# Optimization experiments

Measured on AMD Instinct MI355X. Metric: run time of the kernel, lower is better.

## Reference

```python
import jax, jax.numpy as jnp
import numpy as np

N_MOTIF_PER_CLASS = 8
N_CLASS = 16
N_MOTIF = N_MOTIF_PER_CLASS * N_CLASS
TEMPERATURE = 0.2
TAU = 0.99
K2 = 32
EPS = 1e-4


def setup_inputs() -> dict:
    key = jax.random.key(0)
    k1, k2, k3 = jax.random.split(key, 3)
    N, H = 32768, 1024
    z = jax.random.normal(k1, (N, H), dtype=jnp.float32)
    Motif_Vector = jax.random.normal(k2, (N_MOTIF, H), dtype=jnp.float32)
    y = jax.random.randint(k3, (N,), 0, N_CLASS, dtype=jnp.int64)
    return {"z": z, "Motif_Vector": Motif_Vector, "y": y}


def euclidean_1(X, M):
    # squared euclidean distance via GEMM, then log-ratio similarity
    xp = X @ M.T                                     # [N, n_motif]
    distance = (-2.0 * xp
                + jnp.sum(X * X, axis=1, keepdims=True)
                + jnp.sum(M * M, axis=1)[None, :])
    similarity = jnp.log((distance + 1.0) / (distance + EPS))
    return similarity, distance


def reference(z, Motif_Vector, y):
    similarity, distance = euclidean_1(z, Motif_Vector)

    # mapping: motif j belongs to class j // n_motif_per_class
    motif_class = jnp.arange(N_MOTIF) // N_MOTIF_PER_CLASS   # [n_motif]
    true_motifs = (y[:, None] == motif_class[None, :])       # [N, n_motif]

    # contrastive loss (exact torch math: exp(sim/T), max over positives,
    # sum over negatives)
    sims = jnp.exp(similarity / TEMPERATURE)
    sim_pos = jnp.max(jnp.where(true_motifs, sims, -jnp.inf), axis=1)
    sim_neg_sum = jnp.sum(jnp.where(true_motifs, 0.0, sims), axis=1)
    loss = -jnp.mean(jnp.log(sim_pos / (sim_neg_sum + sim_pos)))

    # update_motif (update_type='topk', weighted_mean=False):
    # torch passes `distance` into filter_similar_graph and argsorts
    # descending, i.e. selects the K2 LARGEST distances among same-class
    # samples (faithful to source).
    masked = jnp.where(true_motifs.T, distance.T, -jnp.inf)  # [n_motif, N]
    _, idx = jax.lax.top_k(masked, K2)                       # [n_motif, K2]
    selected = z[idx]                                        # [n_motif, K2, H]
    new_motif = jnp.mean(selected, axis=1)                   # weights = 1/K2
    new_M = TAU * Motif_Vector + (1.0 - TAU) * new_motif

    return loss, new_M
```

## Files before the change

kernel.cpp:

```cpp
#include <hip/hip_runtime.h>
#include <cstdint>
#include <cmath>

#define NROWS 32768
#define HD    1024
#define NMOT  128
#define NCLS  16
#define KSEL  32
#define EPSV  1e-4f

typedef __attribute__((ext_vector_type(4))) float  f32x4;
typedef __attribute__((ext_vector_type(8))) __bf16 bf16x8;
typedef __attribute__((ext_vector_type(4))) __bf16 bf16x4;
typedef unsigned long long u64;

#define WS_MN   64
#define WS_MVBF 256
#define WS_CD   65792
#define WS_S1K  327936
#define WS_CL   459008
#define WS_CCNT 524544
#define CAPC    256

static __device__ __forceinline__ float dot4(float4 v) {
    return v.x * v.x + v.y * v.y + v.z * v.z + v.w * v.w;
}

static __device__ __forceinline__ bf16x4 cvt4(float4 v) {
    bf16x4 t;
    t[0] = (__bf16)v.x; t[1] = (__bf16)v.y; t[2] = (__bf16)v.z; t[3] = (__bf16)v.w;
    return t;
}

static __device__ __forceinline__ u64 pack_key(float v, int idx) {
    unsigned int b = __float_as_uint(v);
    unsigned int mo = (b & 0x80000000u) ? ~b : (b | 0x80000000u);
    unsigned int khi = ~mo;
    return ((u64)khi << 32) | (unsigned int)idx;
}

__global__ __launch_bounds__(256) void prep_k(const float* __restrict__ mv,
                                              const int* __restrict__ y,
                                              float* __restrict__ wsf,
                                              __bf16* __restrict__ mvbf,
                                              int* __restrict__ clist,
                                              int* __restrict__ ccnt) {
    const int b = blockIdx.x;
    const int tid = threadIdx.x;
    if (b < NMOT) {
        const int k = tid * 4;
        float4 v = *(const float4*)&mv[(size_t)b * HD + k];
        *(bf16x4*)&mvbf[(size_t)b * HD + k] = cvt4(v);
        float s = dot4(v);
#pragma unroll
        for (int o = 1; o < 64; o <<= 1) s += __shfl_xor(s, o, 64);
        __shared__ float red[4];
        if ((tid & 63) == 0) red[tid >> 6] = s;
        __syncthreads();
        if (tid == 0) {
            wsf[WS_MN + b] = red[0] + red[1] + red[2] + red[3];
            if (b == 0) wsf[0] = 0.f;
        }
    } else {
        __shared__ int cnt;
        const int lid = b - NMOT;
        const int cls = lid >> 4, chunk = lid & 15;
        const int lane = tid & 63;
        if (tid == 0) cnt = 0;
        __syncthreads();
        const int base = chunk * 2048;
#pragma unroll
        for (int t = 0; t < 8; ++t) {
            const int i = base + t * 256 + tid;
            const bool pred = (y[i] == cls);
            const u64 m = __ballot(pred);
            int wbase = 0;
            if (lane == 0 && m) wbase = atomicAdd(&cnt, (int)__popcll(m));
            wbase = __shfl(wbase, 0, 64);
            if (pred) {
                const int p = wbase + (int)__popcll(m & ((1ull << lane) - 1ull));
                if (p < CAPC) clist[lid * CAPC + p] = i;
            }
        }
        __syncthreads();
        if (tid == 0) ccnt[lid] = cnt < CAPC ? cnt : CAPC;
    }
}

#define BM 64
#define BN 128
#define BK 32
#define NS (HD / BK)
#define SA 40

__global__ __launch_bounds__(256, 2) void gemm_fused(
    const float* __restrict__ z, const __bf16* __restrict__ mvbf,
    const float* __restrict__ mn, float* __restrict__ cd,
    const int* __restrict__ y, float* __restrict__ lossAcc) {
    __shared__ __bf16 As[2][BM * SA];
    __shared__ __bf16 Bs[2][BN * SA];
    __shared__ float  szn[BM];
    __shared__ int    ly[BM];
    __shared__ float  spm[2][BM];
    __shared__ float  sns[2][BM];

    const int tid  = threadIdx.x;
    const int row0 = blockIdx.x * BM;
    const int lane = tid & 63;
    const int wave = tid >> 6;
    const int wr   = wave >> 1;
    const int wc   = wave & 1;
    const int l15  = lane & 15;
    const int quad = lane >> 4;

    const int sq = tid & 7;
    const int sr = tid >> 3;
    const int bq = tid & 3;
    const int br = tid >> 2;

    if (tid < BM) ly[tid] = y[row0 + tid];

    f32x4 acc[2][4];
#pragma unroll
    for (int i = 0; i < 2; ++i)
#pragma unroll
        for (int j = 0; j < 4; ++j) acc[i][j] = (f32x4){0.f, 0.f, 0.f, 0.f};

    float zsq0 = 0.f, zsq1 = 0.f;

    const float*  zb = z + (size_t)(row0 + sr) * HD + sq * 4;
    const __bf16* bb = mvbf + (size_t)br * HD + bq * 8;

    float4 ra0[4], ra1[4];
    bf16x8 rb0[4], rb1[4];
#pragma unroll
    for (int s = 0; s < 4; ++s) {
        ra0[s] = *(const float4*)(zb + s * BK);
        ra1[s] = *(const float4*)(zb + s * BK + 32 * HD);
        rb0[s] = *(const bf16x8*)(bb + s * BK);
        rb1[s] = *(const bf16x8*)(bb + s * BK + 64 * HD);
    }
    *(bf16x4*)&As[0][sr * SA + sq * 4]        = cvt4(ra0[0]);
    *(bf16x4*)&As[0][(sr + 32) * SA + sq * 4] = cvt4(ra1[0]);
    *(bf16x8*)&Bs[0][br * SA + bq * 8]        = rb0[0];
    *(bf16x8*)&Bs[0][(br + 64) * SA + bq * 8] = rb1[0];
    zsq0 += dot4(ra0[0]); zsq1 += dot4(ra1[0]);
    ra0[0] = *(const float4*)(zb + 4 * BK);
    ra1[0] = *(const float4*)(zb + 4 * BK + 32 * HD);
    rb0[0] = *(const bf16x8*)(bb + 4 * BK);
    rb1[0] = *(const bf16x8*)(bb + 4 * BK + 64 * HD);
    __syncthreads();

    for (int it = 0; it < NS / 4; ++it) {
#pragma unroll
        for (int u = 0; u < 4; ++u) {
            const int kt = it * 4 + u;
            const int rbuf = kt & 1;
            const int ko = quad * 8;
            bf16x8 af[2], bfr[4];
#pragma unroll
            for (int i = 0; i < 2; ++i)
                af[i] = *(const bf16x8*)&As[rbuf][(wr * 32 + i * 16 + l15) * SA + ko];
#pragma unroll
            for (int j = 0; j < 4; ++j)
                bfr[j] = *(const bf16x8*)&Bs[rbuf][(wc * 64 + j * 16 + l15) * SA + ko];
            if (kt + 1 < NS) {
                const int w = (kt + 1) & 1;
                const int s = (kt + 1) & 3;
                *(bf16x4*)&As[w][sr * SA + sq * 4]        = cvt4(ra0[s]);
                *(bf16x4*)&As[w][(sr + 32) * SA + sq * 4] = cvt4(ra1[s]);
                *(bf16x8*)&Bs[w][br * SA + bq * 8]        = rb0[s];
                *(bf16x8*)&Bs[w][(br + 64) * SA + bq * 8] = rb1[s];
                zsq0 += dot4(ra0[s]); zsq1 += dot4(ra1[s]);
                if (kt + 5 < NS) {
                    const float*  zn = zb + (kt + 5) * BK;
                    const __bf16* bn = bb + (kt + 5) * BK;
                    ra0[s] = *(const float4*)(zn);
                    ra1[s] = *(const float4*)(zn + 32 * HD);
                    rb0[s] = *(const bf16x8*)(bn);
                    rb1[s] = *(const bf16x8*)(bn + 64 * HD);
                }
            }
#pragma unroll
            for (int i = 0; i < 2; ++i)
#pragma unroll
                for (int j = 0; j < 4; ++j)
                    acc[i][j] = __builtin_amdgcn_mfma_f32_16x16x32_bf16(
                        af[i], bfr[j], acc[i][j], 0, 0, 0);
            __syncthreads();
        }
    }

#pragma unroll
    for (int o = 1; o < 8; o <<= 1) {
        zsq0 += __shfl_xor(zsq0, o, 64);
        zsq1 += __shfl_xor(zsq1, o, 64);
    }
    if (sq == 0) { szn[sr] = zsq0; szn[sr + 32] = zsq1; }
    __syncthreads();

    f32x4 znv[2];
    int rcls[2][4];
#pragma unroll
    for (int i = 0; i < 2; ++i) {
        znv[i] = *(const f32x4*)&szn[wr * 32 + i * 16 + quad * 4];
#pragma unroll
        for (int reg = 0; reg < 4; ++reg)
            rcls[i][reg] = ly[wr * 32 + i * 16 + quad * 4 + reg];
    }
    float pm[2][4], ns[2][4];
#pragma unroll
    for (int i = 0; i < 2; ++i)
#pragma unroll
        for (int reg = 0; reg < 4; ++reg) { pm[i][reg] = 0.f; ns[i][reg] = 0.f; }

#pragma unroll
    for (int j = 0; j < 4; ++j) {
        const int c = wc * 64 + j * 16 + l15;
        const float mc = mn[c];
        const int ccls = c >> 3;
#pragma unroll
        for (int i = 0; i < 2; ++i) {
#pragma unroll
            for (int reg = 0; reg < 4; ++reg) {
                const int row = wr * 32 + i * 16 + quad * 4 + reg;
                float d = znv[i][reg] + mc - 2.f * acc[i][j][reg];
                float r = (d + 1.0f) * __builtin_amdgcn_rcpf(d + EPSV);
                float r2 = r * r;
                float s = r2 * r2 * r;
                if (ccls == rcls[i][reg]) {
                    pm[i][reg] = fmaxf(pm[i][reg], s);
                    cd[(size_t)(row0 + row) * 8 + (c & 7)] = d;
                } else {
                    ns[i][reg] += s;
                }
            }
        }
    }
#pragma unroll
    for (int o = 1; o < 16; o <<= 1) {
#pragma unroll
        for (int i = 0; i < 2; ++i)
#pragma unroll
            for (int reg = 0; reg < 4; ++reg) {
                pm[i][reg] = fmaxf(pm[i][reg], __shfl_xor(pm[i][reg], o, 64));
                ns[i][reg] += __shfl_xor(ns[i][reg], o, 64);
            }
    }
    if (l15 == 0) {
#pragma unroll
        for (int i = 0; i < 2; ++i)
#pragma unroll
            for (int reg = 0; reg < 4; ++reg) {
                const int row = wr * 32 + i * 16 + quad * 4 + reg;
                spm[wc][row] = pm[i][reg];
                sns[wc][row] = ns[i][reg];
            }
    }
    __syncthreads();
    if (tid < BM) {
        float p = fmaxf(spm[0][tid], spm[1][tid]);
        float nsum = sns[0][tid] + sns[1][tid];
        float li = logf((nsum + p) / p);
#pragma unroll
        for (int o = 1; o < 64; o <<= 1) li += __shfl_xor(li, o, 64);
        if (tid == 0) atomicAdd(lossAcc, li);
    }
}

__global__ __launch_bounds__(256) void sel1_k(const int* __restrict__ clist,
                                              const int* __restrict__ ccnt,
                                              const float* __restrict__ cd,
                                              u64* __restrict__ s1k) {
    __shared__ u64 keys[256];

    const int bid = blockIdx.x;
    const int j = bid >> 4, chunk = bid & 15;
    const int cls = j >> 3, m8 = j & 7;
    const int lid = cls * 16 + chunk;
    const int tid = threadIdx.x;

    const int n = ccnt[lid];
    u64 key = ~0ull;
    if (tid < n) {
        const int idx = clist[lid * CAPC + tid];
        key = pack_key(cd[(size_t)idx * 8 + m8], idx);
    }
    keys[tid] = key;
    __syncthreads();

    for (int k = 2; k <= 256; k <<= 1) {
        for (int jj = k >> 1; jj > 0; jj >>= 1) {
            if (tid < 128) {
                const int i  = ((tid & ~(jj - 1)) << 1) | (tid & (jj - 1));
                const int ix = i | jj;
                const u64 A = keys[i], B = keys[ix];
                const bool up = ((i & k) == 0);
                if ((A > B) == up) { keys[i] = B; keys[ix] = A; }
            }
            __syncthreads();
        }
    }
    if (tid < KSEL) s1k[(size_t)j * 512 + chunk * KSEL + tid] = keys[tid];
}

__global__ __launch_bounds__(256) void merge_k(
    const float* __restrict__ z, const float* __restrict__ mv,
    const u64* __restrict__ s1k, const float* __restrict__ lossAcc,
    float* __restrict__ out) {
    __shared__ u64 keys[512];
    __shared__ int sel[KSEL];

    const int b = blockIdx.x;
    const int j = b >> 2, q = b & 3;
    const int tid = threadIdx.x;
    keys[tid]       = s1k[(size_t)j * 512 + tid];
    keys[tid + 256] = s1k[(size_t)j * 512 + 256 + tid];
    __syncthreads();

    for (int k = 2; k <= 512; k <<= 1) {
        for (int jj = k >> 1; jj > 0; jj >>= 1) {
            const int i  = ((tid & ~(jj - 1)) << 1) | (tid & (jj - 1));
            const int ix = i | jj;
            const u64 A = keys[i], B = keys[ix];
            const bool up = ((i & k) == 0);
            if ((A > B) == up) { keys[i] = B; keys[ix] = A; }
            __syncthreads();
        }
    }
    if (tid < KSEL) sel[tid] = (int)(keys[tid] & 0xFFFFFFFFu);
    __syncthreads();

    const int h = q * 256 + tid;
    float s = 0.f;
#pragma unroll 8
    for (int r = 0; r < KSEL; ++r) s += z[(size_t)sel[r] * HD + h];
    out[1 + (size_t)j * HD + h] =
        0.99f * mv[(size_t)j * HD + h] + 0.01f * (s * (1.0f / KSEL));
    if (b == 0 && tid == 0) out[0] = lossAcc[0] * (1.0f / NROWS);
}

extern "C" void kernel_launch(void* const* d_in, const int* in_sizes, int n_in,
                              void* d_out, int out_size, void* d_ws, size_t ws_size,
                              hipStream_t stream) {
    const float* z  = (const float*)d_in[0];
    const float* mv = (const float*)d_in[1];
    const int*   y  = (const int*)d_in[2];
    float* out = (float*)d_out;
    float* wsf = (float*)d_ws;
    float*  mn    = wsf + WS_MN;
    __bf16* mvbf  = (__bf16*)(wsf + WS_MVBF);
    float*  cd    = wsf + WS_CD;
    u64*    s1k   = (u64*)(wsf + WS_S1K);
    int*    clist = (int*)(wsf + WS_CL);
    int*    ccnt  = (int*)(wsf + WS_CCNT);

    hipLaunchKernelGGL(prep_k,     dim3(NMOT + 256), dim3(256), 0, stream,
                       mv, y, wsf, mvbf, clist, ccnt);
    hipLaunchKernelGGL(gemm_fused, dim3(NROWS / BM), dim3(256), 0, stream,
                       z, mvbf, mn, cd, y, wsf);
    hipLaunchKernelGGL(sel1_k,     dim3(NMOT * 16),  dim3(256), 0, stream,
                       clist, ccnt, cd, s1k);
    hipLaunchKernelGGL(merge_k,    dim3(NMOT * 4),   dim3(256), 0, stream,
                       z, mv, s1k, wsf, out);
}
```

Baseline: 231.0 us.

## Fuse prep, selection and merge kernels into two launches with last-block merge

Removes the prep kernel: the GEMM now reads fp32 motif vectors directly, converting them to bf16 in-loop and computing motif norms itself. Class-list building moves into the selection kernel, and the final merge is done by the last-arriving block per motif via an atomic counter. The loss is reduced deterministically from per-block partials instead of a global atomic. This cuts launches from four to two, at the cost of every GEMM block redundantly converting and normalising the full motif matrix, plus 16x redundant y scans in the selection kernel.

```diff
diff --git a/kernel.cpp b/kernel.cpp
--- a/kernel.cpp
+++ b/kernel.cpp
@@ -14,12 +14,10 @@
 typedef __attribute__((ext_vector_type(4))) __bf16 bf16x4;
 typedef unsigned long long u64;
 
-#define WS_MN   64
-#define WS_MVBF 256
-#define WS_CD   65792
-#define WS_S1K  327936
-#define WS_CL   459008
-#define WS_CCNT 524544
+#define WS_LP   0
+#define WS_MC   512
+#define WS_S1K  1024
+#define WS_CD   132096
 #define CAPC    256
 
 static __device__ __forceinline__ float dot4(float4 v) {
@@ -29,6 +27,13 @@
 static __device__ __forceinline__ bf16x4 cvt4(float4 v) {
     bf16x4 t;
     t[0] = (__bf16)v.x; t[1] = (__bf16)v.y; t[2] = (__bf16)v.z; t[3] = (__bf16)v.w;
+    return t;
+}
+
+static __device__ __forceinline__ bf16x8 cvt8(float4 a, float4 b) {
+    bf16x8 t;
+    t[0] = (__bf16)a.x; t[1] = (__bf16)a.y; t[2] = (__bf16)a.z; t[3] = (__bf16)a.w;
+    t[4] = (__bf16)b.x; t[5] = (__bf16)b.y; t[6] = (__bf16)b.z; t[7] = (__bf16)b.w;
     return t;
 }
 
@@ -39,54 +44,6 @@
     return ((u64)khi << 32) | (unsigned int)idx;
 }
 
-__global__ __launch_bounds__(256) void prep_k(const float* __restrict__ mv,
-                                              const int* __restrict__ y,
-                                              float* __restrict__ wsf,
-                                              __bf16* __restrict__ mvbf,
-                                              int* __restrict__ clist,
-                                              int* __restrict__ ccnt) {
-    const int b = blockIdx.x;
-    const int tid = threadIdx.x;
-    if (b < NMOT) {
-        const int k = tid * 4;
-        float4 v = *(const float4*)&mv[(size_t)b * HD + k];
-        *(bf16x4*)&mvbf[(size_t)b * HD + k] = cvt4(v);
-        float s = dot4(v);
-#pragma unroll
-        for (int o = 1; o < 64; o <<= 1) s += __shfl_xor(s, o, 64);
-        __shared__ float red[4];
-        if ((tid & 63) == 0) red[tid >> 6] = s;
-        __syncthreads();
-        if (tid == 0) {
-            wsf[WS_MN + b] = red[0] + red[1] + red[2] + red[3];
-            if (b == 0) wsf[0] = 0.f;
-        }
-    } else {
-        __shared__ int cnt;
-        const int lid = b - NMOT;
-        const int cls = lid >> 4, chunk = lid & 15;
-        const int lane = tid & 63;
-        if (tid == 0) cnt = 0;
-        __syncthreads();
-        const int base = chunk * 2048;
-#pragma unroll
-        for (int t = 0; t < 8; ++t) {
-            const int i = base + t * 256 + tid;
-            const bool pred = (y[i] == cls);
-            const u64 m = __ballot(pred);
-            int wbase = 0;
-            if (lane == 0 && m) wbase = atomicAdd(&cnt, (int)__popcll(m));
-            wbase = __shfl(wbase, 0, 64);
-            if (pred) {
-                const int p = wbase + (int)__popcll(m & ((1ull << lane) - 1ull));
-                if (p < CAPC) clist[lid * CAPC + p] = i;
-            }
-        }
-        __syncthreads();
-        if (tid == 0) ccnt[lid] = cnt < CAPC ? cnt : CAPC;
-    }
-}
-
 #define BM 64
 #define BN 128
 #define BK 32
@@ -94,12 +51,13 @@
 #define SA 40
 
 __global__ __launch_bounds__(256, 2) void gemm_fused(
-    const float* __restrict__ z, const __bf16* __restrict__ mvbf,
-    const float* __restrict__ mn, float* __restrict__ cd,
-    const int* __restrict__ y, float* __restrict__ lossAcc) {
+    const float* __restrict__ z, const float* __restrict__ mv,
+    float* __restrict__ cd, const int* __restrict__ y,
+    float* __restrict__ lossP, int* __restrict__ mcnt) {
     __shared__ __bf16 As[2][BM * SA];
     __shared__ __bf16 Bs[2][BN * SA];
     __shared__ float  szn[BM];
+    __shared__ float  smn[BN];
     __shared__ int    ly[BM];
     __shared__ float  spm[2][BM];
     __shared__ float  sns[2][BM];
@@ -118,6 +76,7 @@
     const int bq = tid & 3;
     const int br = tid >> 2;
 
+    if (blockIdx.x == 0 && tid < NMOT) mcnt[tid] = 0;
     if (tid < BM) ly[tid] = y[row0 + tid];
 
     f32x4 acc[2][4];
@@ -127,28 +86,38 @@
         for (int j = 0; j < 4; ++j) acc[i][j] = (f32x4){0.f, 0.f, 0.f, 0.f};
 
     float zsq0 = 0.f, zsq1 = 0.f;
-
-    const float*  zb = z + (size_t)(row0 + sr) * HD + sq * 4;
-    const __bf16* bb = mvbf + (size_t)br * HD + bq * 8;
+    float msq0 = 0.f, msq1 = 0.f;
+
+    const float* zb = z  + (size_t)(row0 + sr) * HD + sq * 4;
+    const float* bb = mv + (size_t)br * HD + bq * 8;
 
     float4 ra0[4], ra1[4];
-    bf16x8 rb0[4], rb1[4];
+    float4 rb0[2][2], rb1[2][2];
 #pragma unroll
     for (int s = 0; s < 4; ++s) {
         ra0[s] = *(const float4*)(zb + s * BK);
         ra1[s] = *(const float4*)(zb + s * BK + 32 * HD);
-        rb0[s] = *(const bf16x8*)(bb + s * BK);
-        rb1[s] = *(const bf16x8*)(bb + s * BK + 64 * HD);
+    }
+#pragma unroll
+    for (int s = 0; s < 2; ++s) {
+        rb0[s][0] = *(const float4*)(bb + s * BK);
+        rb0[s][1] = *(const float4*)(bb + s * BK + 4);
+        rb1[s][0] = *(const float4*)(bb + s * BK + 64 * HD);
+        rb1[s][1] = *(const float4*)(bb + s * BK + 64 * HD + 4);
     }
     *(bf16x4*)&As[0][sr * SA + sq * 4]        = cvt4(ra0[0]);
     *(bf16x4*)&As[0][(sr + 32) * SA + sq * 4] = cvt4(ra1[0]);
-    *(bf16x8*)&Bs[0][br * SA + bq * 8]        = rb0[0];
-    *(bf16x8*)&Bs[0][(br + 64) * SA + bq * 8] = rb1[0];
+    *(bf16x8*)&Bs[0][br * SA + bq * 8]        = cvt8(rb0[0][0], rb0[0][1]);
+    *(bf16x8*)&Bs[0][(br + 64) * SA + bq * 8] = cvt8(rb1[0][0], rb1[0][1]);
     zsq0 += dot4(ra0[0]); zsq1 += dot4(ra1[0]);
+    msq0 += dot4(rb0[0][0]) + dot4(rb0[0][1]);
+    msq1 += dot4(rb1[0][0]) + dot4(rb1[0][1]);
     ra0[0] = *(const float4*)(zb + 4 * BK);
     ra1[0] = *(const float4*)(zb + 4 * BK + 32 * HD);
-    rb0[0] = *(const bf16x8*)(bb + 4 * BK);
-    rb1[0] = *(const bf16x8*)(bb + 4 * BK + 64 * HD);
+    rb0[0][0] = *(const float4*)(bb + 2 * BK);
+    rb0[0][1] = *(const float4*)(bb + 2 * BK + 4);
+    rb1[0][0] = *(const float4*)(bb + 2 * BK + 64 * HD);
+    rb1[0][1] = *(const float4*)(bb + 2 * BK + 64 * HD + 4);
     __syncthreads();
 
     for (int it = 0; it < NS / 4; ++it) {
@@ -165,20 +134,27 @@
             for (int j = 0; j < 4; ++j)
                 bfr[j] = *(const bf16x8*)&Bs[rbuf][(wc * 64 + j * 16 + l15) * SA + ko];
             if (kt + 1 < NS) {
-                const int w = (kt + 1) & 1;
-                const int s = (kt + 1) & 3;
-                *(bf16x4*)&As[w][sr * SA + sq * 4]        = cvt4(ra0[s]);
-                *(bf16x4*)&As[w][(sr + 32) * SA + sq * 4] = cvt4(ra1[s]);
-                *(bf16x8*)&Bs[w][br * SA + bq * 8]        = rb0[s];
-                *(bf16x8*)&Bs[w][(br + 64) * SA + bq * 8] = rb1[s];
-                zsq0 += dot4(ra0[s]); zsq1 += dot4(ra1[s]);
+                const int w  = (kt + 1) & 1;
+                const int sA = (kt + 1) & 3;
+                const int sB = (kt + 1) & 1;
+                *(bf16x4*)&As[w][sr * SA + sq * 4]        = cvt4(ra0[sA]);
+                *(bf16x4*)&As[w][(sr + 32) * SA + sq * 4] = cvt4(ra1[sA]);
+                *(bf16x8*)&Bs[w][br * SA + bq * 8]        = cvt8(rb0[sB][0], rb0[sB][1]);
+                *(bf16x8*)&Bs[w][(br + 64) * SA + bq * 8] = cvt8(rb1[sB][0], rb1[sB][1]);
+                zsq0 += dot4(ra0[sA]); zsq1 += dot4(ra1[sA]);
+                msq0 += dot4(rb0[sB][0]) + dot4(rb0[sB][1]);
+                msq1 += dot4(rb1[sB][0]) + dot4(rb1[sB][1]);
                 if (kt + 5 < NS) {
-                    const float*  zn = zb + (kt + 5) * BK;
-                    const __bf16* bn = bb + (kt + 5) * BK;
-                    ra0[s] = *(const float4*)(zn);
-                    ra1[s] = *(const float4*)(zn + 32 * HD);
-                    rb0[s] = *(const bf16x8*)(bn);
-                    rb1[s] = *(const bf16x8*)(bn + 64 * HD);
+                    const float* zn = zb + (kt + 5) * BK;
+                    ra0[sA] = *(const float4*)(zn);
+                    ra1[sA] = *(const float4*)(zn + 32 * HD);
+                }
+                if (kt + 3 < NS) {
+                    const float* bn = bb + (kt + 3) * BK;
+                    rb0[sB][0] = *(const float4*)(bn);
+                    rb0[sB][1] = *(const float4*)(bn + 4);
+                    rb1[sB][0] = *(const float4*)(bn + 64 * HD);
+                    rb1[sB][1] = *(const float4*)(bn + 64 * HD + 4);
                 }
             }
 #pragma unroll
@@ -197,6 +173,12 @@
         zsq1 += __shfl_xor(zsq1, o, 64);
     }
     if (sq == 0) { szn[sr] = zsq0; szn[sr + 32] = zsq1; }
+#pragma unroll
+    for (int o = 1; o < 4; o <<= 1) {
+        msq0 += __shfl_xor(msq0, o, 64);
+        msq1 += __shfl_xor(msq1, o, 64);
+    }
+    if (bq == 0) { smn[br] = msq0; smn[br + 64] = msq1; }
     __syncthreads();
 
     f32x4 znv[2];
@@ -217,7 +199,7 @@
 #pragma unroll
     for (int j = 0; j < 4; ++j) {
         const int c = wc * 64 + j * 16 + l15;
-        const float mc = mn[c];
+        const float mc = smn[c];
         const int ccls = c >> 3;
 #pragma unroll
         for (int i = 0; i < 2; ++i) {
@@ -264,31 +246,54 @@
         float li = logf((nsum + p) / p);
 #pragma unroll
         for (int o = 1; o < 64; o <<= 1) li += __shfl_xor(li, o, 64);
-        if (tid == 0) atomicAdd(lossAcc, li);
-    }
-}
-
-__global__ __launch_bounds__(256) void sel1_k(const int* __restrict__ clist,
-                                              const int* __restrict__ ccnt,
-                                              const float* __restrict__ cd,
-                                              u64* __restrict__ s1k) {
-    __shared__ u64 keys[256];
-
-    const int bid = blockIdx.x;
-    const int j = bid >> 4, chunk = bid & 15;
+        if (tid == 0) lossP[blockIdx.x] = li;
+    }
+}
+
+__global__ __launch_bounds__(256) void selmerge_k(
+    const int* __restrict__ y, const float* __restrict__ cd,
+    const float* __restrict__ z, const float* __restrict__ mv,
+    const float* __restrict__ lossP, u64* __restrict__ s1k,
+    int* __restrict__ mcnt, float* __restrict__ out) {
+    __shared__ u64 keys[512];
+    __shared__ int clist[CAPC];
+    __shared__ int sel[KSEL];
+    __shared__ int cnt;
+    __shared__ int winflag;
+    __shared__ float redf[4];
+
+    const int b = blockIdx.x;
+    const int j = b >> 4, chunk = b & 15;
     const int cls = j >> 3, m8 = j & 7;
-    const int lid = cls * 16 + chunk;
     const int tid = threadIdx.x;
-
-    const int n = ccnt[lid];
+    const int lane = tid & 63;
+
+    if (tid == 0) cnt = 0;
+    __syncthreads();
+    const int base = chunk * 2048;
+#pragma unroll
+    for (int t = 0; t < 8; ++t) {
+        const int i = base + t * 256 + tid;
+        const bool pred = (y[i] == cls);
+        const u64 m = __ballot(pred);
+        int wbase = 0;
+        if (lane == 0 && m) wbase = atomicAdd(&cnt, (int)__popcll(m));
+        wbase = __shfl(wbase, 0, 64);
+        if (pred) {
+            const int p = wbase + (int)__popcll(m & ((1ull << lane) - 1ull));
+            if (p < CAPC) clist[p] = i;
+        }
+    }
+    __syncthreads();
+    const int n = cnt < CAPC ? cnt : CAPC;
+
     u64 key = ~0ull;
     if (tid < n) {
-        const int idx = clist[lid * CAPC + tid];
+        const int idx = clist[tid];
         key = pack_key(cd[(size_t)idx * 8 + m8], idx);
     }
     keys[tid] = key;
     __syncthreads();
-
     for (int k = 2; k <= 256; k <<= 1) {
         for (int jj = k >> 1; jj > 0; jj >>= 1) {
             if (tid < 128) {
@@ -302,22 +307,30 @@
         }
     }
     if (tid < KSEL) s1k[(size_t)j * 512 + chunk * KSEL + tid] = keys[tid];
-}
-
-__global__ __launch_bounds__(256) void merge_k(
-    const float* __restrict__ z, const float* __restrict__ mv,
-    const u64* __restrict__ s1k, const float* __restrict__ lossAcc,
-    float* __restrict__ out) {
-    __shared__ u64 keys[512];
-    __shared__ int sel[KSEL];
-
-    const int b = blockIdx.x;
-    const int j = b >> 2, q = b & 3;
-    const int tid = threadIdx.x;
+
+    if (b == 0) {
+        float s = lossP[tid] + lossP[tid + 256];
+#pragma unroll
+        for (int o = 1; o < 64; o <<= 1) s += __shfl_xor(s, o, 64);
+        if (lane == 0) redf[tid >> 6] = s;
+    }
+
+    __threadfence();
+    __syncthreads();
+    if (b == 0 && tid == 0)
+        out[0] = (redf[0] + redf[1] + redf[2] + redf[3]) * (1.0f / NROWS);
+    if (tid == 0) {
+        int old = __hip_atomic_fetch_add(&mcnt[j], 1, __ATOMIC_ACQ_REL,
+                                         __HIP_MEMORY_SCOPE_AGENT);
+        winflag = (old == 15) ? 1 : 0;
+    }
+    __syncthreads();
+    if (!winflag) return;
+    __threadfence();
+
     keys[tid]       = s1k[(size_t)j * 512 + tid];
     keys[tid + 256] = s1k[(size_t)j * 512 + 256 + tid];
     __syncthreads();
-
     for (int k = 2; k <= 512; k <<= 1) {
         for (int jj = k >> 1; jj > 0; jj >>= 1) {
             const int i  = ((tid & ~(jj - 1)) << 1) | (tid & (jj - 1));
@@ -331,13 +344,18 @@
     if (tid < KSEL) sel[tid] = (int)(keys[tid] & 0xFFFFFFFFu);
     __syncthreads();
 
-    const int h = q * 256 + tid;
-    float s = 0.f;
+    const int h = tid * 4;
+    float4 s = {0.f, 0.f, 0.f, 0.f};
 #pragma unroll 8
-    for (int r = 0; r < KSEL; ++r) s += z[(size_t)sel[r] * HD + h];
-    out[1 + (size_t)j * HD + h] =
-        0.99f * mv[(size_t)j * HD + h] + 0.01f * (s * (1.0f / KSEL));
-    if (b == 0 && tid == 0) out[0] = lossAcc[0] * (1.0f / NROWS);
+    for (int r = 0; r < KSEL; ++r) {
+        const float4 v = *(const float4*)&z[(size_t)sel[r] * HD + h];
+        s.x += v.x; s.y += v.y; s.z += v.z; s.w += v.w;
+    }
+    const float4 m4 = *(const float4*)&mv[(size_t)j * HD + h];
+    out[1 + (size_t)j * HD + h + 0] = 0.99f * m4.x + 0.01f * (s.x * (1.0f / KSEL));
+    out[1 + (size_t)j * HD + h + 1] = 0.99f * m4.y + 0.01f * (s.y * (1.0f / KSEL));
+    out[1 + (size_t)j * HD + h + 2] = 0.99f * m4.z + 0.01f * (s.z * (1.0f / KSEL));
+    out[1 + (size_t)j * HD + h + 3] = 0.99f * m4.w + 0.01f * (s.w * (1.0f / KSEL));
 }
 
 extern "C" void kernel_launch(void* const* d_in, const int* in_sizes, int n_in,
@@ -348,19 +366,13 @@
     const int*   y  = (const int*)d_in[2];
     float* out = (float*)d_out;
     float* wsf = (float*)d_ws;
-    float*  mn    = wsf + WS_MN;
-    __bf16* mvbf  = (__bf16*)(wsf + WS_MVBF);
-    float*  cd    = wsf + WS_CD;
-    u64*    s1k   = (u64*)(wsf + WS_S1K);
-    int*    clist = (int*)(wsf + WS_CL);
-    int*    ccnt  = (int*)(wsf + WS_CCNT);
-
-    hipLaunchKernelGGL(prep_k,     dim3(NMOT + 256), dim3(256), 0, stream,
-                       mv, y, wsf, mvbf, clist, ccnt);
+    float* lossP = wsf + WS_LP;
+    int*   mcnt  = (int*)(wsf + WS_MC);
+    u64*   s1k   = (u64*)(wsf + WS_S1K);
+    float* cd    = wsf + WS_CD;
+
     hipLaunchKernelGGL(gemm_fused, dim3(NROWS / BM), dim3(256), 0, stream,
-                       z, mvbf, mn, cd, y, wsf);
-    hipLaunchKernelGGL(sel1_k,     dim3(NMOT * 16),  dim3(256), 0, stream,
-                       clist, ccnt, cd, s1k);
-    hipLaunchKernelGGL(merge_k,    dim3(NMOT * 4),   dim3(256), 0, stream,
-                       z, mv, s1k, wsf, out);
-}
+                       z, mv, cd, y, lossP, mcnt);
+    hipLaunchKernelGGL(selmerge_k, dim3(NMOT * 16), dim3(256), 0, stream,
+                       y, cd, z, mv, lossP, s1k, mcnt, out);
+}
```

Measured after the change: 424.7 us. 1.84x slower.
